# Kernel optimization log

Measured on AMD Instinct MI355X. Metric: run time of the kernel, lower is better.

The kernel has to match this reference:

```python
import jax, jax.numpy as jnp
import numpy as np

N_IMG, C_IN, H, W = 8, 8, 136, 200
N_INST = 512
CHANNELS = 8
STRIDE = 8
MASK_OUT_STRIDE = 4
# sizes_of_interest + [last*2], per __init__
SOI = jnp.asarray([64.0, 128.0, 256.0, 512.0, 1024.0, 2048.0], dtype=jnp.float32)
W_NUMS = [(C_IN + 2) * CHANNELS, CHANNELS * CHANNELS, CHANNELS]
B_NUMS = [CHANNELS, CHANNELS, 1]
N_PARAMS = sum(W_NUMS) + sum(B_NUMS)  # 169


def compute_locations(h, w, stride):
    # matches adet compute_locations: centers of stride-sized cells, (x, y)
    shifts_x = jnp.arange(w, dtype=jnp.float32) * stride + stride // 2
    shifts_y = jnp.arange(h, dtype=jnp.float32) * stride + stride // 2
    ys, xs = jnp.meshgrid(shifts_y, shifts_x, indexing='ij')
    return jnp.stack([xs.reshape(-1), ys.reshape(-1)], axis=1)  # [h*w, 2]


def bilinear_up_align_corners(x, out_h, out_w):
    # x: [n, h, w]; F.interpolate(mode='bilinear', align_corners=True)
    n, h, w = x.shape
    ys = jnp.linspace(0.0, h - 1.0, out_h)
    xs = jnp.linspace(0.0, w - 1.0, out_w)
    y0 = jnp.floor(ys).astype(jnp.int32)
    x0 = jnp.floor(xs).astype(jnp.int32)
    y1 = jnp.minimum(y0 + 1, h - 1)
    x1 = jnp.minimum(x0 + 1, w - 1)
    wy = (ys - y0.astype(jnp.float32))[None, :, None]
    wx = (xs - x0.astype(jnp.float32))[None, None, :]
    top = x[:, y0, :]
    bot = x[:, y1, :]
    row0 = top[:, :, x0] * (1.0 - wx) + top[:, :, x1] * wx
    row1 = bot[:, :, x0] * (1.0 - wx) + bot[:, :, x1] * wx
    return row0 * (1.0 - wy) + row1 * wy


def dice_coefficient(x, target):
    eps = 1e-5
    n = x.shape[0]
    x = x.reshape(n, -1)
    target = target.reshape(n, -1)
    intersection = jnp.sum(x * target, axis=1)
    union = jnp.sum(x * x, axis=1) + jnp.sum(target * target, axis=1) + eps
    return 1.0 - 2.0 * intersection / union


def setup_inputs() -> dict:
    key = jax.random.key(0)
    ks = jax.random.split(key, 6)
    mask_feats = jax.random.normal(ks[0], (N_IMG, C_IN, H, W), jnp.float32)
    mask_head_params = jax.random.normal(ks[1], (N_INST, N_PARAMS), jnp.float32) * 0.1
    instance_locations = jax.random.uniform(ks[2], (N_INST, 2), jnp.float32) * jnp.asarray(
        [W * STRIDE, H * STRIDE], dtype=jnp.float32)
    gt_masks = (jax.random.uniform(ks[3], (N_INST, 2 * H, 2 * W), jnp.float32) > 0.5).astype(jnp.float32)
    im_inds = jax.random.randint(ks[4], (N_INST,), 0, N_IMG, jnp.int32)
    fpn_levels = jax.random.randint(ks[5], (N_INST,), 0, 5, jnp.int32)
    return {
        'mask_feats': mask_feats,
        'mask_head_params': mask_head_params,
        'instance_locations': instance_locations,
        'gt_masks': gt_masks,
        'im_inds': im_inds,
        'fpn_levels': fpn_levels,
        'mask_feat_stride': 8,
    }


def reference(mask_feats, mask_head_params, instance_locations, gt_masks, im_inds, fpn_levels, mask_feat_stride):
    n_inst = mask_head_params.shape[0]
    # relative coordinates: instance center minus every grid location, / size-of-interest
    locations = compute_locations(H, W, mask_feat_stride)          # [H*W, 2]
    rel = instance_locations[:, None, :] - locations[None, :, :]   # [n, H*W, 2]
    rel = jnp.transpose(rel, (0, 2, 1)) / SOI[fpn_levels][:, None, None]
    rel = rel.reshape(n_inst, 2, H, W)
    feats = mask_feats[im_inds]                                    # gather [n, C_IN, H, W]
    x = jnp.concatenate([rel, feats], axis=1)                      # [n, C_IN+2, H, W]

    # parse_dynamic_params: split per-instance params into 1x1 conv weights/biases
    splits = np.cumsum(W_NUMS + B_NUMS)[:-1].tolist()
    p = jnp.split(mask_head_params, splits, axis=1)
    w0 = p[0].reshape(n_inst, CHANNELS, C_IN + 2)
    w1 = p[1].reshape(n_inst, CHANNELS, CHANNELS)
    w2 = p[2].reshape(n_inst, 1, CHANNELS)
    b0, b1, b2 = p[3], p[4], p[5]

    # grouped 1x1 convs (groups = n_inst) == per-instance channel GEMM
    x = jax.nn.relu(jnp.einsum('nchw,noc->nohw', x, w0) + b0[:, :, None, None])
    x = jax.nn.relu(jnp.einsum('nchw,noc->nohw', x, w1) + b1[:, :, None, None])
    logits = jnp.einsum('nchw,noc->nohw', x, w2) + b2[:, :, None, None]  # [n, 1, H, W]

    up = mask_feat_stride // MASK_OUT_STRIDE
    logits_up = bilinear_up_align_corners(logits[:, 0], H * up, W * up)
    scores = jax.nn.sigmoid(logits_up)
    loss = dice_coefficient(scores, gt_masks)                      # [n]
    return loss
```

## Files before the change

### kernel.cpp

```cpp
#include <hip/hip_runtime.h>
#include <math.h>

#define NIMG 8
#define CIN 8
#define Hh 136
#define Ww 200
#define OH 272
#define OW 400
#define NINST 512
#define NPAR 169
#define TROWS 34
#define NTILES 8
#define LROWS 19

__global__ __launch_bounds__(256) void dmh_main(
    const float* __restrict__ feats,
    const float* __restrict__ pars,
    const float* __restrict__ iloc,
    const float* __restrict__ gt,
    const int* __restrict__ iminds,
    const int* __restrict__ lvls,
    float* __restrict__ acc)
{
    __shared__ float slog[LROWS * Ww];
    __shared__ float sred[12];

    const int n    = blockIdx.y;
    const int tile = blockIdx.x;
    const int tid  = threadIdx.x;

    const float* pp = pars + n * NPAR;
    float w0[80], w1[64], w2[8], b0[8], b1[8], b2;
#pragma unroll
    for (int i = 0; i < 80; i++) w0[i] = pp[i];
#pragma unroll
    for (int i = 0; i < 64; i++) w1[i] = pp[80 + i];
#pragma unroll
    for (int i = 0; i < 8; i++)  w2[i] = pp[144 + i];
#pragma unroll
    for (int i = 0; i < 8; i++)  b0[i] = pp[152 + i];
#pragma unroll
    for (int i = 0; i < 8; i++)  b1[i] = pp[160 + i];
    b2 = pp[168];

    const float ix = iloc[2 * n + 0];
    const float iy = iloc[2 * n + 1];
    const int   im = iminds[n];
    const float invsoi = 1.0f / (float)(64 << lvls[n]);

    const float sy = 135.0f / 271.0f;
    const float sx = 199.0f / 399.0f;

    const int oy0 = tile * TROWS;
    const int ly0 = (int)((float)oy0 * sy);
    int lyL = (int)((float)(oy0 + TROWS - 1) * sy) + 1;
    if (lyL > Hh - 1) lyL = Hh - 1;
    const int lycnt = lyL - ly0 + 1;

    const float* fb0 = feats + (size_t)im * (CIN * Hh * Ww);
    const int npix = lycnt * Ww;
    for (int i = tid; i < npix; i += 256) {
        const int yy = i / Ww;
        const int x  = i - yy * Ww;
        const int y  = ly0 + yy;
        const float r0 = (ix - (float)(x * 8 + 4)) * invsoi;
        const float r1 = (iy - (float)(y * 8 + 4)) * invsoi;
        const float* fb = fb0 + y * Ww + x;
        float f[8];
#pragma unroll
        for (int c = 0; c < 8; c++) f[c] = fb[c * (Hh * Ww)];
        float h[8];
#pragma unroll
        for (int o = 0; o < 8; o++) {
            float a = b0[o] + w0[o * 10 + 0] * r0 + w0[o * 10 + 1] * r1;
#pragma unroll
            for (int c = 0; c < 8; c++) a += w0[o * 10 + 2 + c] * f[c];
            h[o] = fmaxf(a, 0.0f);
        }
        float g[8];
#pragma unroll
        for (int o = 0; o < 8; o++) {
            float a = b1[o];
#pragma unroll
            for (int c = 0; c < 8; c++) a += w1[o * 8 + c] * h[c];
            g[o] = fmaxf(a, 0.0f);
        }
        float lg = b2;
#pragma unroll
        for (int c = 0; c < 8; c++) lg += w2[c] * g[c];
        slog[i] = lg;
    }
    __syncthreads();

    float aI = 0.0f, aS = 0.0f, aT = 0.0f;
    const float* gtn = gt + (size_t)n * (OH * OW) + (size_t)oy0 * OW;
    for (int i = tid; i < TROWS * OW; i += 256) {
        const int ry = i / OW;
        const int ox = i - ry * OW;
        const int oy = oy0 + ry;
        const float ysf = (float)oy * sy;
        const float xsf = (float)ox * sx;
        int y0 = (int)ysf, x0 = (int)xsf;
        const float wy = ysf - (float)y0;
        const float wx = xsf - (float)x0;
        int y1 = (y0 + 1 > Hh - 1) ? (Hh - 1) : (y0 + 1);
        int x1 = (x0 + 1 > Ww - 1) ? (Ww - 1) : (x0 + 1);
        int r0i = y0 - ly0, r1i = y1 - ly0;
        r0i = r0i < 0 ? 0 : (r0i > lycnt - 1 ? lycnt - 1 : r0i);
        r1i = r1i < 0 ? 0 : (r1i > lycnt - 1 ? lycnt - 1 : r1i);
        const float v00 = slog[r0i * Ww + x0];
        const float v01 = slog[r0i * Ww + x1];
        const float v10 = slog[r1i * Ww + x0];
        const float v11 = slog[r1i * Ww + x1];
        const float top = v00 * (1.0f - wx) + v01 * wx;
        const float bot = v10 * (1.0f - wx) + v11 * wx;
        const float v   = top * (1.0f - wy) + bot * wy;
        const float s   = __fdividef(1.0f, 1.0f + __expf(-v));
        const float t   = gtn[i];
        aI += s * t;
        aS += s * s;
        aT += t;
    }

#pragma unroll
    for (int off = 32; off > 0; off >>= 1) {
        aI += __shfl_down(aI, off, 64);
        aS += __shfl_down(aS, off, 64);
        aT += __shfl_down(aT, off, 64);
    }
    const int wv = tid >> 6;
    if ((tid & 63) == 0) {
        sred[wv * 3 + 0] = aI;
        sred[wv * 3 + 1] = aS;
        sred[wv * 3 + 2] = aT;
    }
    __syncthreads();
    if (tid == 0) {
        const float I = sred[0] + sred[3] + sred[6] + sred[9];
        const float S = sred[1] + sred[4] + sred[7] + sred[10];
        const float T = sred[2] + sred[5] + sred[8] + sred[11];
        atomicAdd(&acc[n * 3 + 0], I);
        atomicAdd(&acc[n * 3 + 1], S);
        atomicAdd(&acc[n * 3 + 2], T);
    }
}

__global__ __launch_bounds__(256) void dmh_fin(const float* __restrict__ acc,
                                               float* __restrict__ out)
{
    const int i = blockIdx.x * 256 + threadIdx.x;
    if (i < NINST) {
        const float I = acc[i * 3 + 0];
        const float S = acc[i * 3 + 1];
        const float T = acc[i * 3 + 2];
        out[i] = 1.0f - 2.0f * I / (S + T + 1e-5f);
    }
}

extern "C" void kernel_launch(void* const* d_in, const int* in_sizes, int n_in,
                              void* d_out, int out_size, void* d_ws, size_t ws_size,
                              hipStream_t stream) {
    const float* feats  = (const float*)d_in[0];
    const float* pars   = (const float*)d_in[1];
    const float* iloc   = (const float*)d_in[2];
    const float* gt     = (const float*)d_in[3];
    const int*   iminds = (const int*)d_in[4];
    const int*   lvls   = (const int*)d_in[5];
    float* acc = (float*)d_ws;

    hipMemsetAsync(acc, 0, NINST * 3 * sizeof(float), stream);
    dim3 grid(NTILES, NINST);
    dmh_main<<<grid, 256, 0, stream>>>(feats, pars, iloc, gt, iminds, lvls, acc);
    dmh_fin<<<(NINST + 255) / 256, 256, 0, stream>>>(acc, (float*)d_out);
}
```

Measured before the change: 470.8 us.

## Vectorize feature loads, fold relative-coordinate math into precomputed coefficients, pair gt loads

Each thread now loads four adjacent pixels per channel with float4 and computes four logits, writing them to shared memory as a float4. The relative-coordinate terms of the first conv layer are folded into per-output affine coefficients, so each pixel's coordinate contribution costs two FMAs. The upsample/dice loop handles two output pixels per iteration, reading the ground truth with float2 and using the lerp form of bilinear interpolation. Launch bounds now request 2 blocks per CU, which may raise register pressure given the per-thread weight arrays.

```diff
diff --git a/kernel.cpp b/kernel.cpp
--- a/kernel.cpp
+++ b/kernel.cpp
@@ -5,6 +5,7 @@
 #define CIN 8
 #define Hh 136
 #define Ww 200
+#define HW (Hh * Ww)
 #define OH 272
 #define OW 400
 #define NINST 512
@@ -13,7 +14,7 @@
 #define NTILES 8
 #define LROWS 19
 
-__global__ __launch_bounds__(256) void dmh_main(
+__global__ __launch_bounds__(256, 2) void dmh_main(
     const float* __restrict__ feats,
     const float* __restrict__ pars,
     const float* __restrict__ iloc,
@@ -29,24 +30,30 @@
     const int tile = blockIdx.x;
     const int tid  = threadIdx.x;
 
-    const float* pp = pars + n * NPAR;
-    float w0[80], w1[64], w2[8], b0[8], b1[8], b2;
-#pragma unroll
-    for (int i = 0; i < 80; i++) w0[i] = pp[i];
-#pragma unroll
-    for (int i = 0; i < 64; i++) w1[i] = pp[80 + i];
-#pragma unroll
-    for (int i = 0; i < 8; i++)  w2[i] = pp[144 + i];
-#pragma unroll
-    for (int i = 0; i < 8; i++)  b0[i] = pp[152 + i];
-#pragma unroll
-    for (int i = 0; i < 8; i++)  b1[i] = pp[160 + i];
-    b2 = pp[168];
-
     const float ix = iloc[2 * n + 0];
     const float iy = iloc[2 * n + 1];
     const int   im = iminds[n];
     const float invsoi = 1.0f / (float)(64 << lvls[n]);
+
+    const float* pp = pars + n * NPAR;
+    float Wf[64], w1[64], w2[8], b1[8], A0[8], Ax[8], Ay[8], b2;
+#pragma unroll
+    for (int o = 0; o < 8; o++) {
+        const float wx0 = pp[o * 10 + 0];
+        const float wy0 = pp[o * 10 + 1];
+        Ax[o] = -8.0f * invsoi * wx0;
+        Ay[o] = -8.0f * invsoi * wy0;
+        A0[o] = pp[152 + o] + wx0 * (ix - 4.0f) * invsoi + wy0 * (iy - 4.0f) * invsoi;
+#pragma unroll
+        for (int c = 0; c < 8; c++) Wf[o * 8 + c] = pp[o * 10 + 2 + c];
+    }
+#pragma unroll
+    for (int i = 0; i < 64; i++) w1[i] = pp[80 + i];
+#pragma unroll
+    for (int i = 0; i < 8; i++)  w2[i] = pp[144 + i];
+#pragma unroll
+    for (int i = 0; i < 8; i++)  b1[i] = pp[160 + i];
+    b2 = pp[168];
 
     const float sy = 135.0f / 271.0f;
     const float sx = 199.0f / 399.0f;
@@ -57,69 +64,91 @@
     if (lyL > Hh - 1) lyL = Hh - 1;
     const int lycnt = lyL - ly0 + 1;
 
-    const float* fb0 = feats + (size_t)im * (CIN * Hh * Ww);
-    const int npix = lycnt * Ww;
-    for (int i = tid; i < npix; i += 256) {
-        const int yy = i / Ww;
-        const int x  = i - yy * Ww;
+    const float* fb0 = feats + (size_t)im * (CIN * HW);
+    const int nquad = lycnt * (Ww / 4);
+    for (int q = tid; q < nquad; q += 256) {
+        const int yy = q / 50;
+        const int xq = (q - yy * 50) * 4;
         const int y  = ly0 + yy;
-        const float r0 = (ix - (float)(x * 8 + 4)) * invsoi;
-        const float r1 = (iy - (float)(y * 8 + 4)) * invsoi;
-        const float* fb = fb0 + y * Ww + x;
-        float f[8];
-#pragma unroll
-        for (int c = 0; c < 8; c++) f[c] = fb[c * (Hh * Ww)];
-        float h[8];
-#pragma unroll
-        for (int o = 0; o < 8; o++) {
-            float a = b0[o] + w0[o * 10 + 0] * r0 + w0[o * 10 + 1] * r1;
-#pragma unroll
-            for (int c = 0; c < 8; c++) a += w0[o * 10 + 2 + c] * f[c];
-            h[o] = fmaxf(a, 0.0f);
+        const float yf = (float)y;
+        const float* fb = fb0 + y * Ww + xq;
+        float f[8][4];
+#pragma unroll
+        for (int c = 0; c < 8; c++) {
+            const float4 t = *reinterpret_cast<const float4*>(fb + c * HW);
+            f[c][0] = t.x; f[c][1] = t.y; f[c][2] = t.z; f[c][3] = t.w;
         }
-        float g[8];
-#pragma unroll
-        for (int o = 0; o < 8; o++) {
-            float a = b1[o];
-#pragma unroll
-            for (int c = 0; c < 8; c++) a += w1[o * 8 + c] * h[c];
-            g[o] = fmaxf(a, 0.0f);
+        float pre[8];
+#pragma unroll
+        for (int o = 0; o < 8; o++) pre[o] = A0[o] + Ay[o] * yf;
+
+        float out4[4];
+#pragma unroll
+        for (int p = 0; p < 4; p++) {
+            const float xf = (float)(xq + p);
+            float h[8];
+#pragma unroll
+            for (int o = 0; o < 8; o++) {
+                float a = pre[o] + Ax[o] * xf;
+#pragma unroll
+                for (int c = 0; c < 8; c++) a += Wf[o * 8 + c] * f[c][p];
+                h[o] = fmaxf(a, 0.0f);
+            }
+            float g[8];
+#pragma unroll
+            for (int o = 0; o < 8; o++) {
+                float a = b1[o];
+#pragma unroll
+                for (int c = 0; c < 8; c++) a += w1[o * 8 + c] * h[c];
+                g[o] = fmaxf(a, 0.0f);
+            }
+            float lg = b2;
+#pragma unroll
+            for (int c = 0; c < 8; c++) lg += w2[c] * g[c];
+            out4[p] = lg;
         }
-        float lg = b2;
-#pragma unroll
-        for (int c = 0; c < 8; c++) lg += w2[c] * g[c];
-        slog[i] = lg;
+        *reinterpret_cast<float4*>(&slog[yy * Ww + xq]) =
+            make_float4(out4[0], out4[1], out4[2], out4[3]);
     }
     __syncthreads();
 
     float aI = 0.0f, aS = 0.0f, aT = 0.0f;
     const float* gtn = gt + (size_t)n * (OH * OW) + (size_t)oy0 * OW;
-    for (int i = tid; i < TROWS * OW; i += 256) {
-        const int ry = i / OW;
-        const int ox = i - ry * OW;
+    for (int g2 = tid; g2 < TROWS * (OW / 2); g2 += 256) {
+        const int ry = g2 / 200;
+        const int gx = (g2 - ry * 200) * 2;
         const int oy = oy0 + ry;
         const float ysf = (float)oy * sy;
-        const float xsf = (float)ox * sx;
-        int y0 = (int)ysf, x0 = (int)xsf;
+        int y0 = (int)ysf;
         const float wy = ysf - (float)y0;
-        const float wx = xsf - (float)x0;
         int y1 = (y0 + 1 > Hh - 1) ? (Hh - 1) : (y0 + 1);
-        int x1 = (x0 + 1 > Ww - 1) ? (Ww - 1) : (x0 + 1);
         int r0i = y0 - ly0, r1i = y1 - ly0;
         r0i = r0i < 0 ? 0 : (r0i > lycnt - 1 ? lycnt - 1 : r0i);
         r1i = r1i < 0 ? 0 : (r1i > lycnt - 1 ? lycnt - 1 : r1i);
-        const float v00 = slog[r0i * Ww + x0];
-        const float v01 = slog[r0i * Ww + x1];
-        const float v10 = slog[r1i * Ww + x0];
-        const float v11 = slog[r1i * Ww + x1];
-        const float top = v00 * (1.0f - wx) + v01 * wx;
-        const float bot = v10 * (1.0f - wx) + v11 * wx;
-        const float v   = top * (1.0f - wy) + bot * wy;
-        const float s   = __fdividef(1.0f, 1.0f + __expf(-v));
-        const float t   = gtn[i];
-        aI += s * t;
-        aS += s * s;
-        aT += t;
+        const float* s0 = &slog[r0i * Ww];
+        const float* s1 = &slog[r1i * Ww];
+
+        const float2 t2 = *reinterpret_cast<const float2*>(gtn + ry * OW + gx);
+        const float tval[2] = { t2.x, t2.y };
+#pragma unroll
+        for (int p = 0; p < 2; p++) {
+            const int ox = gx + p;
+            const float xsf = (float)ox * sx;
+            const int x0 = (int)xsf;
+            const float wx = xsf - (float)x0;
+            const int x1 = (x0 + 1 > Ww - 1) ? (Ww - 1) : (x0 + 1);
+            const float v00 = s0[x0];
+            const float v01 = s0[x1];
+            const float v10 = s1[x0];
+            const float v11 = s1[x1];
+            const float top = v00 + wx * (v01 - v00);
+            const float bot = v10 + wx * (v11 - v10);
+            const float v   = top + wy * (bot - top);
+            const float s   = __fdividef(1.0f, 1.0f + __expf(-v));
+            aI += s * tval[p];
+            aS += s * s;
+            aT += tval[p];
+        }
     }
 
 #pragma unroll
```

New measurement: 578.2 us. 1.23x slower.

## Split fused kernel into MLP-to-workspace and dice kernels with vectorized loads

Applied to the files above, without the earlier changes.

Splits the fused kernel in two when the workspace is large enough. The first kernel computes per-instance logits once per low-resolution pixel and writes them to global workspace, which removes the halo recomputation across overlapping tiles. It also processes pixel pairs with float2 loads and folds the relative-coordinate terms into precomputed affine coefficients. The second kernel reads tile rows into shared memory, does the upsample, sigmoid and dice sums with float4 gt loads, and writes per-tile partials instead of using atomics. In exchange it adds a round-trip of about 56 MB of logits through global memory and one more launch.

```diff
diff --git a/kernel.cpp b/kernel.cpp
--- a/kernel.cpp
+++ b/kernel.cpp
@@ -5,6 +5,7 @@
 #define CIN 8
 #define Hh 136
 #define Ww 200
+#define HW (Hh * Ww)
 #define OH 272
 #define OW 400
 #define NINST 512
@@ -12,8 +13,201 @@
 #define TROWS 34
 #define NTILES 8
 #define LROWS 19
-
-__global__ __launch_bounds__(256) void dmh_main(
+#define ACHUNKS 16
+#define PAIRS_PER_CHUNK (HW / 2 / ACHUNKS)
+#define LOG_OFF_FLOATS 16384
+#define WS_NEEDED ((size_t)(LOG_OFF_FLOATS + (size_t)NINST * HW) * 4)
+
+__global__ __launch_bounds__(256, 1) void dmh_mlp(
+    const float* __restrict__ feats,
+    const float* __restrict__ pars,
+    const float* __restrict__ iloc,
+    const int* __restrict__ iminds,
+    const int* __restrict__ lvls,
+    float* __restrict__ logits)
+{
+    const int n     = blockIdx.y;
+    const int chunk = blockIdx.x;
+    const int tid   = threadIdx.x;
+
+    const float ix = iloc[2 * n + 0];
+    const float iy = iloc[2 * n + 1];
+    const int   im = iminds[n];
+    const float invsoi = 1.0f / (float)(64 << lvls[n]);
+
+    const float* pp = pars + n * NPAR;
+    float Wf[64], w1[64], w2[8], b1[8], A0[8], Ax[8], Ay[8], b2;
+#pragma unroll
+    for (int o = 0; o < 8; o++) {
+        const float wx0 = pp[o * 10 + 0];
+        const float wy0 = pp[o * 10 + 1];
+        Ax[o] = -8.0f * invsoi * wx0;
+        Ay[o] = -8.0f * invsoi * wy0;
+        A0[o] = pp[152 + o] + (wx0 * (ix - 4.0f) + wy0 * (iy - 4.0f)) * invsoi;
+#pragma unroll
+        for (int c = 0; c < 8; c++) Wf[o * 8 + c] = pp[o * 10 + 2 + c];
+    }
+#pragma unroll
+    for (int i = 0; i < 64; i++) w1[i] = pp[80 + i];
+#pragma unroll
+    for (int i = 0; i < 8; i++)  w2[i] = pp[144 + i];
+#pragma unroll
+    for (int i = 0; i < 8; i++)  b1[i] = pp[160 + i];
+    b2 = pp[168];
+
+    const float* fb0 = feats + (size_t)im * (CIN * HW);
+    float* lgn = logits + (size_t)n * HW;
+
+    const int base = chunk * PAIRS_PER_CHUNK;
+    const int end  = base + PAIRS_PER_CHUNK;
+    for (int pr = base + tid; pr < end; pr += 256) {
+        const int yy = pr / 100;
+        const int xp = (pr - yy * 100) * 2;
+        const float yf = (float)yy;
+        const float* fb = fb0 + yy * Ww + xp;
+        float f[8][2];
+#pragma unroll
+        for (int c = 0; c < 8; c++) {
+            const float2 t = *reinterpret_cast<const float2*>(fb + c * HW);
+            f[c][0] = t.x; f[c][1] = t.y;
+        }
+        float pre[8];
+#pragma unroll
+        for (int o = 0; o < 8; o++) pre[o] = A0[o] + Ay[o] * yf;
+
+        float o2[2];
+#pragma unroll
+        for (int p = 0; p < 2; p++) {
+            const float xf = (float)(xp + p);
+            float h[8];
+#pragma unroll
+            for (int o = 0; o < 8; o++) {
+                float a = pre[o] + Ax[o] * xf;
+#pragma unroll
+                for (int c = 0; c < 8; c++) a += Wf[o * 8 + c] * f[c][p];
+                h[o] = fmaxf(a, 0.0f);
+            }
+            float g[8];
+#pragma unroll
+            for (int o = 0; o < 8; o++) {
+                float a = b1[o];
+#pragma unroll
+                for (int c = 0; c < 8; c++) a += w1[o * 8 + c] * h[c];
+                g[o] = fmaxf(a, 0.0f);
+            }
+            float lg = b2;
+#pragma unroll
+            for (int c = 0; c < 8; c++) lg += w2[c] * g[c];
+            o2[p] = lg;
+        }
+        *reinterpret_cast<float2*>(lgn + yy * Ww + xp) = make_float2(o2[0], o2[1]);
+    }
+}
+
+__global__ __launch_bounds__(256) void dmh_dice(
+    const float* __restrict__ logits,
+    const float* __restrict__ gt,
+    float* __restrict__ part)
+{
+    __shared__ float slog[LROWS * Ww];
+    __shared__ float sred[12];
+
+    const int n    = blockIdx.y;
+    const int tile = blockIdx.x;
+    const int tid  = threadIdx.x;
+
+    const float sy = 135.0f / 271.0f;
+    const float sx = 199.0f / 399.0f;
+
+    const int oy0 = tile * TROWS;
+    const int ly0 = (int)((float)oy0 * sy);
+    int lyL = (int)((float)(oy0 + TROWS - 1) * sy) + 1;
+    if (lyL > Hh - 1) lyL = Hh - 1;
+    const int lycnt = lyL - ly0 + 1;
+
+    const float* lg = logits + (size_t)n * HW + ly0 * Ww;
+    const int nfl = lycnt * Ww;
+    for (int i = 4 * tid; i < nfl; i += 1024) {
+        *reinterpret_cast<float4*>(&slog[i]) = *reinterpret_cast<const float4*>(lg + i);
+    }
+    __syncthreads();
+
+    float aI = 0.0f, aS = 0.0f, aT = 0.0f;
+    const float* gtn = gt + (size_t)n * (OH * OW) + (size_t)oy0 * OW;
+    for (int g4 = tid; g4 < TROWS * (OW / 4); g4 += 256) {
+        const int ry = g4 / 100;
+        const int gx = (g4 - ry * 100) * 4;
+        const int oy = oy0 + ry;
+        const float ysf = (float)oy * sy;
+        const int y0 = (int)ysf;
+        const float wy = ysf - (float)y0;
+        const int y1 = (y0 + 1 > Hh - 1) ? (Hh - 1) : (y0 + 1);
+        int r0i = y0 - ly0, r1i = y1 - ly0;
+        r0i = r0i < 0 ? 0 : (r0i > lycnt - 1 ? lycnt - 1 : r0i);
+        r1i = r1i < 0 ? 0 : (r1i > lycnt - 1 ? lycnt - 1 : r1i);
+        const float* s0 = &slog[r0i * Ww];
+        const float* s1 = &slog[r1i * Ww];
+
+        const float4 t4 = *reinterpret_cast<const float4*>(gtn + ry * OW + gx);
+        const float tv[4] = { t4.x, t4.y, t4.z, t4.w };
+#pragma unroll
+        for (int p = 0; p < 4; p++) {
+            const int ox = gx + p;
+            const float xsf = (float)ox * sx;
+            const int x0 = (int)xsf;
+            const float wx = xsf - (float)x0;
+            const int x1 = (x0 + 1 > Ww - 1) ? (Ww - 1) : (x0 + 1);
+            const float v00 = s0[x0];
+            const float v01 = s0[x1];
+            const float v10 = s1[x0];
+            const float v11 = s1[x1];
+            const float top = v00 + wx * (v01 - v00);
+            const float bot = v10 + wx * (v11 - v10);
+            const float v   = top + wy * (bot - top);
+            const float s   = __fdividef(1.0f, 1.0f + __expf(-v));
+            aI += s * tv[p];
+            aS += s * s;
+            aT += tv[p];
+        }
+    }
+
+#pragma unroll
+    for (int off = 32; off > 0; off >>= 1) {
+        aI += __shfl_down(aI, off, 64);
+        aS += __shfl_down(aS, off, 64);
+        aT += __shfl_down(aT, off, 64);
+    }
+    const int wv = tid >> 6;
+    if ((tid & 63) == 0) {
+        sred[wv * 3 + 0] = aI;
+        sred[wv * 3 + 1] = aS;
+        sred[wv * 3 + 2] = aT;
+    }
+    __syncthreads();
+    if (tid == 0) {
+        float* pt = part + (size_t)(n * NTILES + tile) * 3;
+        pt[0] = sred[0] + sred[3] + sred[6] + sred[9];
+        pt[1] = sred[1] + sred[4] + sred[7] + sred[10];
+        pt[2] = sred[2] + sred[5] + sred[8] + sred[11];
+    }
+}
+
+__global__ __launch_bounds__(256) void dmh_fin2(const float* __restrict__ part,
+                                                float* __restrict__ out)
+{
+    const int i = blockIdx.x * 256 + threadIdx.x;
+    if (i < NINST) {
+        float I = 0.0f, S = 0.0f, T = 0.0f;
+#pragma unroll
+        for (int t = 0; t < NTILES; t++) {
+            const float* pt = part + (size_t)(i * NTILES + t) * 3;
+            I += pt[0]; S += pt[1]; T += pt[2];
+        }
+        out[i] = 1.0f - 2.0f * I / (S + T + 1e-5f);
+    }
+}
+
+__global__ __launch_bounds__(256) void dmh_fused(
     const float* __restrict__ feats,
     const float* __restrict__ pars,
     const float* __restrict__ iloc,
@@ -24,11 +218,7 @@
 {
     __shared__ float slog[LROWS * Ww];
     __shared__ float sred[12];
-
-    const int n    = blockIdx.y;
-    const int tile = blockIdx.x;
-    const int tid  = threadIdx.x;
-
+    const int n = blockIdx.y, tile = blockIdx.x, tid = threadIdx.x;
     const float* pp = pars + n * NPAR;
     float w0[80], w1[64], w2[8], b0[8], b1[8], b2;
 #pragma unroll
@@ -42,22 +232,16 @@
 #pragma unroll
     for (int i = 0; i < 8; i++)  b1[i] = pp[160 + i];
     b2 = pp[168];
-
-    const float ix = iloc[2 * n + 0];
-    const float iy = iloc[2 * n + 1];
-    const int   im = iminds[n];
+    const float ix = iloc[2 * n + 0], iy = iloc[2 * n + 1];
+    const int im = iminds[n];
     const float invsoi = 1.0f / (float)(64 << lvls[n]);
-
-    const float sy = 135.0f / 271.0f;
-    const float sx = 199.0f / 399.0f;
-
+    const float sy = 135.0f / 271.0f, sx = 199.0f / 399.0f;
     const int oy0 = tile * TROWS;
     const int ly0 = (int)((float)oy0 * sy);
     int lyL = (int)((float)(oy0 + TROWS - 1) * sy) + 1;
     if (lyL > Hh - 1) lyL = Hh - 1;
     const int lycnt = lyL - ly0 + 1;
-
-    const float* fb0 = feats + (size_t)im * (CIN * Hh * Ww);
+    const float* fb0 = feats + (size_t)im * (CIN * HW);
     const int npix = lycnt * Ww;
     for (int i = tid; i < npix; i += 256) {
         const int yy = i / Ww;
@@ -68,7 +252,7 @@
         const float* fb = fb0 + y * Ww + x;
         float f[8];
 #pragma unroll
-        for (int c = 0; c < 8; c++) f[c] = fb[c * (Hh * Ww)];
+        for (int c = 0; c < 8; c++) f[c] = fb[c * HW];
         float h[8];
 #pragma unroll
         for (int o = 0; o < 8; o++) {
@@ -91,7 +275,6 @@
         slog[i] = lg;
     }
     __syncthreads();
-
     float aI = 0.0f, aS = 0.0f, aT = 0.0f;
     const float* gtn = gt + (size_t)n * (OH * OW) + (size_t)oy0 * OW;
     for (int i = tid; i < TROWS * OW; i += 256) {
@@ -112,16 +295,13 @@
         const float v01 = slog[r0i * Ww + x1];
         const float v10 = slog[r1i * Ww + x0];
         const float v11 = slog[r1i * Ww + x1];
-        const float top = v00 * (1.0f - wx) + v01 * wx;
-        const float bot = v10 * (1.0f - wx) + v11 * wx;
-        const float v   = top * (1.0f - wy) + bot * wy;
+        const float top = v00 + wx * (v01 - v00);
+        const float bot = v10 + wx * (v11 - v10);
+        const float v   = top + wy * (bot - top);
         const float s   = __fdividef(1.0f, 1.0f + __expf(-v));
         const float t   = gtn[i];
-        aI += s * t;
-        aS += s * s;
-        aT += t;
-    }
-
+        aI += s * t; aS += s * s; aT += t;
+    }
 #pragma unroll
     for (int off = 32; off > 0; off >>= 1) {
         aI += __shfl_down(aI, off, 64);
@@ -130,18 +310,13 @@
     }
     const int wv = tid >> 6;
     if ((tid & 63) == 0) {
-        sred[wv * 3 + 0] = aI;
-        sred[wv * 3 + 1] = aS;
-        sred[wv * 3 + 2] = aT;
+        sred[wv * 3 + 0] = aI; sred[wv * 3 + 1] = aS; sred[wv * 3 + 2] = aT;
     }
     __syncthreads();
     if (tid == 0) {
-        const float I = sred[0] + sred[3] + sred[6] + sred[9];
-        const float S = sred[1] + sred[4] + sred[7] + sred[10];
-        const float T = sred[2] + sred[5] + sred[8] + sred[11];
-        atomicAdd(&acc[n * 3 + 0], I);
-        atomicAdd(&acc[n * 3 + 1], S);
-        atomicAdd(&acc[n * 3 + 2], T);
+        atomicAdd(&acc[n * 3 + 0], sred[0] + sred[3] + sred[6] + sred[9]);
+        atomicAdd(&acc[n * 3 + 1], sred[1] + sred[4] + sred[7] + sred[10]);
+        atomicAdd(&acc[n * 3 + 2], sred[2] + sred[5] + sred[8] + sred[11]);
     }
 }
 
@@ -150,10 +325,7 @@
 {
     const int i = blockIdx.x * 256 + threadIdx.x;
     if (i < NINST) {
-        const float I = acc[i * 3 + 0];
-        const float S = acc[i * 3 + 1];
-        const float T = acc[i * 3 + 2];
-        out[i] = 1.0f - 2.0f * I / (S + T + 1e-5f);
+        out[i] = 1.0f - 2.0f * acc[i * 3 + 0] / (acc[i * 3 + 1] + acc[i * 3 + 2] + 1e-5f);
     }
 }
 
@@ -166,10 +338,20 @@
     const float* gt     = (const float*)d_in[3];
     const int*   iminds = (const int*)d_in[4];
     const int*   lvls   = (const int*)d_in[5];
-    float* acc = (float*)d_ws;
-
-    hipMemsetAsync(acc, 0, NINST * 3 * sizeof(float), stream);
-    dim3 grid(NTILES, NINST);
-    dmh_main<<<grid, 256, 0, stream>>>(feats, pars, iloc, gt, iminds, lvls, acc);
-    dmh_fin<<<(NINST + 255) / 256, 256, 0, stream>>>(acc, (float*)d_out);
-}
+
+    if (ws_size >= WS_NEEDED) {
+        float* part   = (float*)d_ws;
+        float* logits = (float*)d_ws + LOG_OFF_FLOATS;
+        dim3 ga(ACHUNKS, NINST);
+        dmh_mlp<<<ga, 256, 0, stream>>>(feats, pars, iloc, iminds, lvls, logits);
+        dim3 gb(NTILES, NINST);
+        dmh_dice<<<gb, 256, 0, stream>>>(logits, gt, part);
+        dmh_fin2<<<(NINST + 255) / 256, 256, 0, stream>>>(part, (float*)d_out);
+    } else {
+        float* acc = (float*)d_ws;
+        hipMemsetAsync(acc, 0, NINST * 3 * sizeof(float), stream);
+        dim3 grid(NTILES, NINST);
+        dmh_fused<<<grid, 256, 0, stream>>>(feats, pars, iloc, gt, iminds, lvls, acc);
+        dmh_fin<<<(NINST + 255) / 256, 256, 0, stream>>>(acc, (float*)d_out);
+    }
+}
```

New measurement: 482.0 us. +2.4%, slower.
